# Kernel optimization log

Measured on AMD Instinct MI355X. Metric: run time of the kernel, lower is better.

Reference implementation:

```python
import jax, jax.numpy as jnp
import numpy as np

N = 100000       # nodes
E = 3200000      # edges (avg degree 32)
IN_F = 256
OUT_F = 128
LRELU_ALPHA = 0.2
EPS = 1e-16


def setup_inputs() -> dict:
    key = jax.random.key(0)
    k1, k2, k3, k4 = jax.random.split(key, 4)
    x = jax.random.normal(k1, (N, IN_F), dtype=jnp.float32)
    edge_index = jax.random.randint(k2, (2, E), 0, N, dtype=jnp.int32)
    # xavier_uniform with gain=calculate_gain('relu')=sqrt(2)
    gain = float(np.sqrt(2.0))
    bw = gain * float(np.sqrt(6.0 / (IN_F + OUT_F)))
    weight = jax.random.uniform(k3, (IN_F, OUT_F), dtype=jnp.float32, minval=-bw, maxval=bw)
    ba = gain * float(np.sqrt(6.0 / (1 + 2 * OUT_F)))
    a = jax.random.uniform(k4, (1, 2 * OUT_F), dtype=jnp.float32, minval=-ba, maxval=ba)
    return {"x": x, "edge_index": edge_index, "weight": weight, "a": a}


def reference(x, edge_index, weight, a):
    src = edge_index[0]
    dst = edge_index[1]
    h = x @ weight                                  # [N, OUT_F]
    # e_edge = a @ cat(h[src], h[dst]) == (h @ a_l)[src] + (h @ a_r)[dst]
    a_l = a[0, :OUT_F]
    a_r = a[0, OUT_F:]
    s_l = h @ a_l                                   # [N]
    s_r = h @ a_r                                   # [N]
    e = s_l[src] + s_r[dst]                         # [E]
    e = jnp.where(e >= 0, e, LRELU_ALPHA * e)       # LeakyReLU
    # segment softmax over src groups
    e_max = jax.ops.segment_max(e, src, num_segments=N)   # [N]
    e_exp = jnp.exp(e - e_max[src])                        # [E]
    denom = jax.ops.segment_sum(e_exp, src, num_segments=N)[src] + EPS
    alpha_e = e_exp / denom                                # [E]
    # out[src] += alpha_e * h[dst]  (sparse A_alpha @ h)
    out = jax.ops.segment_sum(alpha_e[:, None] * h[dst], src, num_segments=N)
    return out
```

## Files before the change

kernel.cpp:

```cpp
#include <hip/hip_runtime.h>

#define GN 100000
#define GE 3200000
#define CAP 128
#define NB 391
#define CHUNK 4096
#define BSTRIDE 9216
#define GBLK 782

typedef __attribute__((ext_vector_type(8))) short bf16x8;
typedef __attribute__((ext_vector_type(4))) float f32x4;

__device__ __forceinline__ unsigned short f2bf(float f) {
    unsigned u = __float_as_uint(f);
    u += 0x7fffu + ((u >> 16) & 1u);
    return (unsigned short)(u >> 16);
}
__device__ __forceinline__ unsigned cvtpk(float lo, float hi) {
    unsigned r;
    asm("v_cvt_pk_bf16_f32 %0, %1, %2" : "=v"(r) : "v"(lo), "v"(hi));
    return r;
}

__global__ __launch_bounds__(256) void wprep_kernel(const float* __restrict__ w,
                                                    unsigned short* __restrict__ wT,
                                                    int* __restrict__ bcursor,
                                                    float* __restrict__ s_l) {
    if (blockIdx.x < 32) {
        int flat4 = blockIdx.x * 256 + threadIdx.x;
        int k  = flat4 >> 5;
        int n4 = (flat4 & 31) * 4;
        float4 v = ((const float4*)w)[flat4];
        wT[(size_t)(n4 + 0) * 256 + k] = f2bf(v.x);
        wT[(size_t)(n4 + 1) * 256 + k] = f2bf(v.y);
        wT[(size_t)(n4 + 2) * 256 + k] = f2bf(v.z);
        wT[(size_t)(n4 + 3) * 256 + k] = f2bf(v.w);
    } else if (blockIdx.x < 34) {
        int j = (blockIdx.x - 32) * 256 + threadIdx.x;
        if (j < NB) bcursor[j] = j * BSTRIDE;
    } else {
        int i = (blockIdx.x - 34) * 256 + threadIdx.x;
        if (i < 2 * GN / 4) {
            float4 z = {0.f, 0.f, 0.f, 0.f};
            ((float4*)s_l)[i] = z;
        }
    }
}

__global__ __launch_bounds__(256) void gemmbin_kernel(const float* __restrict__ x,
                                                      const unsigned short* __restrict__ wT,
                                                      const float* __restrict__ a,
                                                      unsigned short* __restrict__ hq,
                                                      float* __restrict__ s_l,
                                                      float* __restrict__ s_r,
                                                      const int* __restrict__ ei,
                                                      int* __restrict__ bcursor,
                                                      unsigned* __restrict__ binned) {
    __shared__ __align__(16) char smem[30848];
    const int half = blockIdx.x >> 1;
    const int tid = threadIdx.x;

    if ((blockIdx.x & 1) == 0) {
        unsigned short (*As)[128][40] = (unsigned short (*)[128][40])smem;
        const int lane = tid & 63, wid = tid >> 6;
        const int l16  = lane & 15, quad = lane >> 4;
        const int wm   = (wid >> 1) * 64, wn = (wid & 1) * 64;
        const int bm   = half * 128;

        f32x4 acc[4][4] = {};

        const int arow = tid >> 1, ahalf = tid & 1;
        int gr = bm + arow; if (gr >= GN) gr = GN - 1;
        const float* xrow = x + (size_t)gr * 256 + ahalf * 16;

        {
            float4 f0 = *(const float4*)(xrow + 0);
            float4 f1 = *(const float4*)(xrow + 4);
            float4 f2 = *(const float4*)(xrow + 8);
            float4 f3 = *(const float4*)(xrow + 12);
            uint4 u0, u1;
            u0.x = cvtpk(f0.x, f0.y); u0.y = cvtpk(f0.z, f0.w);
            u0.z = cvtpk(f1.x, f1.y); u0.w = cvtpk(f1.z, f1.w);
            u1.x = cvtpk(f2.x, f2.y); u1.y = cvtpk(f2.z, f2.w);
            u1.z = cvtpk(f3.x, f3.y); u1.w = cvtpk(f3.z, f3.w);
            *(uint4*)&As[0][arow][ahalf * 16]     = u0;
            *(uint4*)&As[0][arow][ahalf * 16 + 8] = u1;
        }
        bf16x8 bcur[4];
#pragma unroll
        for (int t = 0; t < 4; ++t)
            bcur[t] = *(const bf16x8*)(wT + (size_t)(wn + t * 16 + l16) * 256 + quad * 8);
        __syncthreads();

#pragma unroll
        for (int ks = 0; ks < 8; ++ks) {
            const int cb = ks & 1;
            bf16x8 bnxt[4];
            uint4 u0, u1;
            if (ks < 7) {
                const int k1 = (ks + 1) * 32;
#pragma unroll
                for (int t = 0; t < 4; ++t)
                    bnxt[t] = *(const bf16x8*)(wT + (size_t)(wn + t * 16 + l16) * 256 + k1 + quad * 8);
                float4 f0 = *(const float4*)(xrow + k1);
                float4 f1 = *(const float4*)(xrow + k1 + 4);
                float4 f2 = *(const float4*)(xrow + k1 + 8);
                float4 f3 = *(const float4*)(xrow + k1 + 12);
                u0.x = cvtpk(f0.x, f0.y); u0.y = cvtpk(f0.z, f0.w);
                u0.z = cvtpk(f1.x, f1.y); u0.w = cvtpk(f1.z, f1.w);
                u1.x = cvtpk(f2.x, f2.y); u1.y = cvtpk(f2.z, f2.w);
                u1.z = cvtpk(f3.x, f3.y); u1.w = cvtpk(f3.z, f3.w);
            }
            bf16x8 af[4];
#pragma unroll
            for (int t = 0; t < 4; ++t)
                af[t] = *(const bf16x8*)&As[cb][wm + t * 16 + l16][quad * 8];
#pragma unroll
            for (int ti = 0; ti < 4; ++ti)
#pragma unroll
                for (int tj = 0; tj < 4; ++tj)
                    acc[ti][tj] = __builtin_amdgcn_mfma_f32_16x16x32_bf16(af[ti], bcur[tj], acc[ti][tj], 0, 0, 0);
            if (ks < 7) {
                *(uint4*)&As[cb ^ 1][arow][ahalf * 16]     = u0;
                *(uint4*)&As[cb ^ 1][arow][ahalf * 16 + 8] = u1;
                __syncthreads();
#pragma unroll
                for (int t = 0; t < 4; ++t) bcur[t] = bnxt[t];
            }
        }

        float alv[4], arv[4];
#pragma unroll
        for (int tj = 0; tj < 4; ++tj) {
            alv[tj] = a[wn + tj * 16 + l16];
            arv[tj] = a[128 + wn + tj * 16 + l16];
        }
#pragma unroll
        for (int ti = 0; ti < 4; ++ti) {
            float slp[4], srp[4];
#pragma unroll
            for (int r = 0; r < 4; ++r) {
                int row = bm + wm + ti * 16 + quad * 4 + r;
                float v0 = acc[ti][0][r], v1 = acc[ti][1][r], v2 = acc[ti][2][r], v3 = acc[ti][3][r];
                if (row < GN) {
                    unsigned short* hp = hq + (size_t)row * 128 + wn + l16;
                    hp[0]  = f2bf(v0);
                    hp[16] = f2bf(v1);
                    hp[32] = f2bf(v2);
                    hp[48] = f2bf(v3);
                }
                slp[r] = v0 * alv[0] + v1 * alv[1] + v2 * alv[2] + v3 * alv[3];
                srp[r] = v0 * arv[0] + v1 * arv[1] + v2 * arv[2] + v3 * arv[3];
            }
#pragma unroll
            for (int off = 1; off < 16; off <<= 1)
#pragma unroll
                for (int r = 0; r < 4; ++r) {
                    slp[r] += __shfl_xor(slp[r], off, 64);
                    srp[r] += __shfl_xor(srp[r], off, 64);
                }
            if (l16 == 0) {
#pragma unroll
                for (int r = 0; r < 4; ++r) {
                    int row = bm + wm + ti * 16 + quad * 4 + r;
                    if (row < GN) {
                        atomicAdd(&s_l[row], slp[r]);
                        atomicAdd(&s_r[row], srp[r]);
                    }
                }
            }
        }
    } else {
        int* h_cnt  = (int*)smem;
        int* h_base = h_cnt + NB;
        int* h_gpos = h_base + NB + 1;
        int* h_cur  = h_gpos + NB;
        unsigned* sbuf = (unsigned*)(h_cur + NB);
        unsigned short* sbkt = (unsigned short*)(sbuf + CHUNK);

        const int base = half * CHUNK;
        const int cnt = min(CHUNK, GE - base);

        int srcv[CHUNK / 256], dstv[CHUNK / 256];
#pragma unroll
        for (int i = 0; i < CHUNK / 256; ++i) {
            int idx = tid + i * 256;
            if (idx < cnt) { srcv[i] = ei[base + idx]; dstv[i] = ei[GE + base + idx]; }
            else srcv[i] = -1;
        }
        for (int j = tid; j < NB; j += 256) h_cnt[j] = 0;
        __syncthreads();
#pragma unroll
        for (int i = 0; i < CHUNK / 256; ++i)
            if (srcv[i] >= 0) atomicAdd(&h_cnt[srcv[i] >> 8], 1);
        __syncthreads();
        if (tid < 64) {
            int carry = 0;
            for (int b0 = 0; b0 < NB; b0 += 64) {
                int idx = b0 + tid;
                int v = (idx < NB) ? h_cnt[idx] : 0;
                int xx = v;
#pragma unroll
                for (int off = 1; off < 64; off <<= 1) {
                    int y = __shfl_up(xx, off, 64);
                    if (tid >= off) xx += y;
                }
                if (idx < NB) h_base[idx] = carry + xx - v;
                carry += __shfl(xx, 63, 64);
            }
            if (tid == 0) h_base[NB] = carry;
        }
        __syncthreads();
        for (int j = tid; j < NB; j += 256) {
            h_cur[j] = h_base[j];
            int c = h_cnt[j];
            if (c) h_gpos[j] = atomicAdd(&bcursor[j], c);
        }
        __syncthreads();
#pragma unroll
        for (int i = 0; i < CHUNK / 256; ++i)
            if (srcv[i] >= 0) {
                int b = srcv[i] >> 8;
                int p = atomicAdd(&h_cur[b], 1);
                sbuf[p] = ((unsigned)(srcv[i] & 255) << 17) | (unsigned)dstv[i];
                sbkt[p] = (unsigned short)b;
            }
        __syncthreads();
        for (int p = tid; p < cnt; p += 256) {
            int b = sbkt[p];
            binned[h_gpos[b] + (p - h_base[b])] = sbuf[p];
        }
    }
}

__global__ __launch_bounds__(1024) void fine_kernel(unsigned* __restrict__ binned,
                                                    const int* __restrict__ bcursor,
                                                    int* __restrict__ rowbeg,
                                                    int* __restrict__ rowend) {
    __shared__ unsigned sedge[BSTRIDE];
    __shared__ int n_cnt[256];
    __shared__ int n_base[256];
    __shared__ int n_cur[256];
    const int b = blockIdx.x;
    const int tid = threadIdx.x;
    const int node0 = b * 256;
    const int nn = min(256, GN - node0);
    const int beg = b * BSTRIDE;
    const int cnt = bcursor[b] - beg;
    if (tid < 256) n_cnt[tid] = 0;
    for (int p = tid; p < cnt; p += 1024) sedge[p] = binned[beg + p];
    __syncthreads();
    for (int p = tid; p < cnt; p += 1024)
        atomicAdd(&n_cnt[sedge[p] >> 17], 1);
    __syncthreads();
    if (tid < 64) {
        int carry = 0;
        for (int b0 = 0; b0 < 256; b0 += 64) {
            int idx = b0 + tid;
            int v = n_cnt[idx];
            int x = v;
#pragma unroll
            for (int off = 1; off < 64; off <<= 1) {
                int y = __shfl_up(x, off, 64);
                if (tid >= off) x += y;
            }
            n_base[idx] = carry + x - v;
            carry += __shfl(x, 63, 64);
        }
    }
    __syncthreads();
    if (tid < nn) {
        rowbeg[node0 + tid] = beg + n_base[tid];
        rowend[node0 + tid] = beg + n_base[tid] + n_cnt[tid];
    }
    if (tid < 256) n_cur[tid] = n_base[tid];
    __syncthreads();
    for (int p = tid; p < cnt; p += 1024) {
        unsigned e = sedge[p];
        int pos = atomicAdd(&n_cur[e >> 17], 1);
        binned[beg + pos] = e & 0x1FFFFu;
    }
}

__global__ __launch_bounds__(256) void aggregate_kernel(const uint4* __restrict__ h4,
                                                        const float* __restrict__ s_l,
                                                        const float* __restrict__ s_r,
                                                        const int* __restrict__ rowbeg,
                                                        const int* __restrict__ rowend,
                                                        const int* __restrict__ adj,
                                                        float* __restrict__ out) {
    __shared__ int   s_dst[4][CAP];
    __shared__ float s_w[4][CAP];
    const int wid = threadIdx.x >> 6, lane = threadIdx.x & 63;
    const int node = blockIdx.x * 4 + wid;
    const int beg = rowbeg[node], end = rowend[node];
    const int deg = end - beg;
    const float sl = s_l[node];

    float m = -1e30f;
    for (int j = lane; j < deg; j += 64) {
        int dst = adj[beg + j];
        float e = sl + s_r[dst];
        e = (e >= 0.f) ? e : 0.2f * e;
        if (j < CAP) { s_dst[wid][j] = dst; s_w[wid][j] = e; }
        m = fmaxf(m, e);
    }
#pragma unroll
    for (int off = 1; off < 64; off <<= 1)
        m = fmaxf(m, __shfl_xor(m, off, 64));
    __syncthreads();

    const int n2 = deg < CAP ? deg : CAP;
    float d = 0.f;
    for (int j = lane; j < n2; j += 64) {
        float w = __expf(s_w[wid][j] - m);
        s_w[wid][j] = w;
        d += w;
    }
    for (int j = CAP + lane; j < deg; j += 64) {
        int dst = adj[beg + j];
        float e = sl + s_r[dst];
        e = (e >= 0.f) ? e : 0.2f * e;
        d += __expf(e - m);
    }
#pragma unroll
    for (int off = 1; off < 64; off <<= 1)
        d += __shfl_xor(d, off, 64);
    const float inv = 1.f / (d + 1e-16f);
    __syncthreads();

    const int fl = lane & 15, grp = lane >> 4;
    f32x4 accA = {0.f, 0.f, 0.f, 0.f}, accB = {0.f, 0.f, 0.f, 0.f};
    int j = 0;
#pragma unroll 2
    for (; j < n2; j += 8) {
        int j0 = j + grp, j1 = j + grp + 4;
        bool a0 = j0 < n2, a1 = j1 < n2;
        int   d0 = s_dst[wid][a0 ? j0 : 0];
        int   d1 = s_dst[wid][a1 ? j1 : 0];
        float w0 = a0 ? s_w[wid][j0] : 0.f;
        float w1 = a1 ? s_w[wid][j1] : 0.f;
        uint4 v0 = h4[(size_t)d0 * 16 + fl];
        uint4 v1 = h4[(size_t)d1 * 16 + fl];
        accA.x += w0 * __uint_as_float(v0.x << 16);
        accA.y += w0 * __uint_as_float(v0.x & 0xffff0000u);
        accA.z += w0 * __uint_as_float(v0.y << 16);
        accA.w += w0 * __uint_as_float(v0.y & 0xffff0000u);
        accB.x += w0 * __uint_as_float(v0.z << 16);
        accB.y += w0 * __uint_as_float(v0.z & 0xffff0000u);
        accB.z += w0 * __uint_as_float(v0.w << 16);
        accB.w += w0 * __uint_as_float(v0.w & 0xffff0000u);
        accA.x += w1 * __uint_as_float(v1.x << 16);
        accA.y += w1 * __uint_as_float(v1.x & 0xffff0000u);
        accA.z += w1 * __uint_as_float(v1.y << 16);
        accA.w += w1 * __uint_as_float(v1.y & 0xffff0000u);
        accB.x += w1 * __uint_as_float(v1.z << 16);
        accB.y += w1 * __uint_as_float(v1.z & 0xffff0000u);
        accB.z += w1 * __uint_as_float(v1.w << 16);
        accB.w += w1 * __uint_as_float(v1.w & 0xffff0000u);
    }
    for (; j < deg; j += 4) {
        int jj = j + grp;
        bool act = jj < deg;
        int dst = act ? adj[beg + jj] : 0;
        float e = sl + s_r[dst];
        e = (e >= 0.f) ? e : 0.2f * e;
        float w = act ? __expf(e - m) : 0.f;
        uint4 v = h4[(size_t)dst * 16 + fl];
        accA.x += w * __uint_as_float(v.x << 16);
        accA.y += w * __uint_as_float(v.x & 0xffff0000u);
        accA.z += w * __uint_as_float(v.y << 16);
        accA.w += w * __uint_as_float(v.y & 0xffff0000u);
        accB.x += w * __uint_as_float(v.z << 16);
        accB.y += w * __uint_as_float(v.z & 0xffff0000u);
        accB.z += w * __uint_as_float(v.w << 16);
        accB.w += w * __uint_as_float(v.w & 0xffff0000u);
    }

#pragma unroll
    for (int off = 16; off < 64; off <<= 1) {
        accA.x += __shfl_xor(accA.x, off, 64);
        accA.y += __shfl_xor(accA.y, off, 64);
        accA.z += __shfl_xor(accA.z, off, 64);
        accA.w += __shfl_xor(accA.w, off, 64);
        accB.x += __shfl_xor(accB.x, off, 64);
        accB.y += __shfl_xor(accB.y, off, 64);
        accB.z += __shfl_xor(accB.z, off, 64);
        accB.w += __shfl_xor(accB.w, off, 64);
    }
    if (lane < 16) {
        float* orow = out + (size_t)node * 128 + fl * 8;
        accA.x *= inv; accA.y *= inv; accA.z *= inv; accA.w *= inv;
        accB.x *= inv; accB.y *= inv; accB.z *= inv; accB.w *= inv;
        *(f32x4*)orow       = accA;
        *(f32x4*)(orow + 4) = accB;
    }
}

extern "C" void kernel_launch(void* const* d_in, const int* in_sizes, int n_in,
                              void* d_out, int out_size, void* d_ws, size_t ws_size,
                              hipStream_t stream) {
    const float* x  = (const float*)d_in[0];
    const int*   ei = (const int*)d_in[1];
    const float* w  = (const float*)d_in[2];
    const float* a  = (const float*)d_in[3];
    float* out = (float*)d_out;

    unsigned short* hq = (unsigned short*)d_ws;
    float* s_l     = (float*)(hq + (size_t)GN * 128);
    float* s_r     = s_l + GN;
    int*   bcursor = (int*)(s_r + GN);
    int*   rowbeg  = bcursor + NB;
    int*   rowend  = rowbeg + GN;
    unsigned* binned = (unsigned*)(rowend + GN);
    unsigned short* wT = (unsigned short*)(binned + (size_t)NB * BSTRIDE);

    wprep_kernel<<<34 + (2 * GN / 4 + 255) / 256, 256, 0, stream>>>(w, wT, bcursor, s_l);
    gemmbin_kernel<<<2 * GBLK, 256, 0, stream>>>(x, wT, a, hq, s_l, s_r, ei, bcursor, binned);
    fine_kernel<<<NB, 1024, 0, stream>>>(binned, bcursor, rowbeg, rowend);
    aggregate_kernel<<<GN / 4, 256, 0, stream>>>((const uint4*)hq, s_l, s_r, rowbeg, rowend,
                                                 (const int*)binned, out);
}
```

Before: 366.5 us.

## Fuse fine-grained CSR sort into aggregation kernel using shared-memory edge lists

```diff
diff --git a/kernel.cpp b/kernel.cpp
--- a/kernel.cpp
+++ b/kernel.cpp
@@ -7,6 +7,7 @@
 #define CHUNK 4096
 #define BSTRIDE 9216
 #define GBLK 782
+#define EPT 18
 
 typedef __attribute__((ext_vector_type(8))) short bf16x8;
 typedef __attribute__((ext_vector_type(4))) float f32x4;
@@ -233,25 +234,35 @@
     }
 }
 
-__global__ __launch_bounds__(1024) void fine_kernel(unsigned* __restrict__ binned,
-                                                    const int* __restrict__ bcursor,
-                                                    int* __restrict__ rowbeg,
-                                                    int* __restrict__ rowend) {
+__global__ __launch_bounds__(512) void aggfine_kernel(const uint4* __restrict__ h4,
+                                                      const float* __restrict__ s_l,
+                                                      const float* __restrict__ s_r,
+                                                      const unsigned* __restrict__ binned,
+                                                      const int* __restrict__ bcursor,
+                                                      float* __restrict__ out) {
     __shared__ unsigned sedge[BSTRIDE];
     __shared__ int n_cnt[256];
     __shared__ int n_base[256];
     __shared__ int n_cur[256];
-    const int b = blockIdx.x;
-    const int tid = threadIdx.x;
+    __shared__ float s_w[8][CAP];
+    const int b    = blockIdx.x;
+    const int tid  = threadIdx.x;
+    const int wid  = tid >> 6, lane = tid & 63;
     const int node0 = b * 256;
-    const int nn = min(256, GN - node0);
-    const int beg = b * BSTRIDE;
-    const int cnt = bcursor[b] - beg;
+    const int beg  = b * BSTRIDE;
+    const int cnt  = min(bcursor[b] - beg, BSTRIDE);
+
+    unsigned ev[EPT];
     if (tid < 256) n_cnt[tid] = 0;
-    for (int p = tid; p < cnt; p += 1024) sedge[p] = binned[beg + p];
     __syncthreads();
-    for (int p = tid; p < cnt; p += 1024)
-        atomicAdd(&n_cnt[sedge[p] >> 17], 1);
+#pragma unroll
+    for (int i = 0; i < EPT; ++i) {
+        int p = tid + i * 512;
+        if (p < cnt) {
+            ev[i] = binned[beg + p];
+            atomicAdd(&n_cnt[ev[i] >> 17], 1);
+        }
+    }
     __syncthreads();
     if (tid < 64) {
         int carry = 0;
@@ -269,131 +280,123 @@
         }
     }
     __syncthreads();
-    if (tid < nn) {
-        rowbeg[node0 + tid] = beg + n_base[tid];
-        rowend[node0 + tid] = beg + n_base[tid] + n_cnt[tid];
-    }
     if (tid < 256) n_cur[tid] = n_base[tid];
     __syncthreads();
-    for (int p = tid; p < cnt; p += 1024) {
-        unsigned e = sedge[p];
-        int pos = atomicAdd(&n_cur[e >> 17], 1);
-        binned[beg + pos] = e & 0x1FFFFu;
-    }
-}
-
-__global__ __launch_bounds__(256) void aggregate_kernel(const uint4* __restrict__ h4,
-                                                        const float* __restrict__ s_l,
-                                                        const float* __restrict__ s_r,
-                                                        const int* __restrict__ rowbeg,
-                                                        const int* __restrict__ rowend,
-                                                        const int* __restrict__ adj,
-                                                        float* __restrict__ out) {
-    __shared__ int   s_dst[4][CAP];
-    __shared__ float s_w[4][CAP];
-    const int wid = threadIdx.x >> 6, lane = threadIdx.x & 63;
-    const int node = blockIdx.x * 4 + wid;
-    const int beg = rowbeg[node], end = rowend[node];
-    const int deg = end - beg;
-    const float sl = s_l[node];
-
-    float m = -1e30f;
-    for (int j = lane; j < deg; j += 64) {
-        int dst = adj[beg + j];
-        float e = sl + s_r[dst];
-        e = (e >= 0.f) ? e : 0.2f * e;
-        if (j < CAP) { s_dst[wid][j] = dst; s_w[wid][j] = e; }
-        m = fmaxf(m, e);
-    }
-#pragma unroll
-    for (int off = 1; off < 64; off <<= 1)
-        m = fmaxf(m, __shfl_xor(m, off, 64));
+#pragma unroll
+    for (int i = 0; i < EPT; ++i) {
+        int p = tid + i * 512;
+        if (p < cnt) {
+            unsigned e = ev[i];
+            int pos = atomicAdd(&n_cur[e >> 17], 1);
+            sedge[pos] = e & 0x1FFFFu;
+        }
+    }
     __syncthreads();
 
-    const int n2 = deg < CAP ? deg : CAP;
-    float d = 0.f;
-    for (int j = lane; j < n2; j += 64) {
-        float w = __expf(s_w[wid][j] - m);
-        s_w[wid][j] = w;
-        d += w;
-    }
-    for (int j = CAP + lane; j < deg; j += 64) {
-        int dst = adj[beg + j];
-        float e = sl + s_r[dst];
-        e = (e >= 0.f) ? e : 0.2f * e;
-        d += __expf(e - m);
-    }
-#pragma unroll
-    for (int off = 1; off < 64; off <<= 1)
-        d += __shfl_xor(d, off, 64);
-    const float inv = 1.f / (d + 1e-16f);
-    __syncthreads();
-
     const int fl = lane & 15, grp = lane >> 4;
-    f32x4 accA = {0.f, 0.f, 0.f, 0.f}, accB = {0.f, 0.f, 0.f, 0.f};
-    int j = 0;
+    for (int k = 0; k < 32; ++k) {
+        const int n = wid * 32 + k;
+        const int node = node0 + n;
+        if (node >= GN) break;
+        const int nb  = n_base[n];
+        const int deg = n_cnt[n];
+        const float sl = s_l[node];
+
+        float m = -1e30f;
+        for (int j = lane; j < deg; j += 64) {
+            int dst = (int)sedge[nb + j];
+            float e = sl + s_r[dst];
+            e = (e >= 0.f) ? e : 0.2f * e;
+            if (j < CAP) s_w[wid][j] = e;
+            m = fmaxf(m, e);
+        }
+#pragma unroll
+        for (int off = 1; off < 64; off <<= 1)
+            m = fmaxf(m, __shfl_xor(m, off, 64));
+
+        const int n2 = deg < CAP ? deg : CAP;
+        float d = 0.f;
+        for (int j = lane; j < n2; j += 64) {
+            float w = __expf(s_w[wid][j] - m);
+            s_w[wid][j] = w;
+            d += w;
+        }
+        for (int j = CAP + lane; j < deg; j += 64) {
+            int dst = (int)sedge[nb + j];
+            float e = sl + s_r[dst];
+            e = (e >= 0.f) ? e : 0.2f * e;
+            d += __expf(e - m);
+        }
+#pragma unroll
+        for (int off = 1; off < 64; off <<= 1)
+            d += __shfl_xor(d, off, 64);
+        const float inv = 1.f / (d + 1e-16f);
+
+        f32x4 accA = {0.f, 0.f, 0.f, 0.f}, accB = {0.f, 0.f, 0.f, 0.f};
+        int j = 0;
 #pragma unroll 2
-    for (; j < n2; j += 8) {
-        int j0 = j + grp, j1 = j + grp + 4;
-        bool a0 = j0 < n2, a1 = j1 < n2;
-        int   d0 = s_dst[wid][a0 ? j0 : 0];
-        int   d1 = s_dst[wid][a1 ? j1 : 0];
-        float w0 = a0 ? s_w[wid][j0] : 0.f;
-        float w1 = a1 ? s_w[wid][j1] : 0.f;
-        uint4 v0 = h4[(size_t)d0 * 16 + fl];
-        uint4 v1 = h4[(size_t)d1 * 16 + fl];
-        accA.x += w0 * __uint_as_float(v0.x << 16);
-        accA.y += w0 * __uint_as_float(v0.x & 0xffff0000u);
-        accA.z += w0 * __uint_as_float(v0.y << 16);
-        accA.w += w0 * __uint_as_float(v0.y & 0xffff0000u);
-        accB.x += w0 * __uint_as_float(v0.z << 16);
-        accB.y += w0 * __uint_as_float(v0.z & 0xffff0000u);
-        accB.z += w0 * __uint_as_float(v0.w << 16);
-        accB.w += w0 * __uint_as_float(v0.w & 0xffff0000u);
-        accA.x += w1 * __uint_as_float(v1.x << 16);
-        accA.y += w1 * __uint_as_float(v1.x & 0xffff0000u);
-        accA.z += w1 * __uint_as_float(v1.y << 16);
-        accA.w += w1 * __uint_as_float(v1.y & 0xffff0000u);
-        accB.x += w1 * __uint_as_float(v1.z << 16);
-        accB.y += w1 * __uint_as_float(v1.z & 0xffff0000u);
-        accB.z += w1 * __uint_as_float(v1.w << 16);
-        accB.w += w1 * __uint_as_float(v1.w & 0xffff0000u);
-    }
-    for (; j < deg; j += 4) {
-        int jj = j + grp;
-        bool act = jj < deg;
-        int dst = act ? adj[beg + jj] : 0;
-        float e = sl + s_r[dst];
-        e = (e >= 0.f) ? e : 0.2f * e;
-        float w = act ? __expf(e - m) : 0.f;
-        uint4 v = h4[(size_t)dst * 16 + fl];
-        accA.x += w * __uint_as_float(v.x << 16);
-        accA.y += w * __uint_as_float(v.x & 0xffff0000u);
-        accA.z += w * __uint_as_float(v.y << 16);
-        accA.w += w * __uint_as_float(v.y & 0xffff0000u);
-        accB.x += w * __uint_as_float(v.z << 16);
-        accB.y += w * __uint_as_float(v.z & 0xffff0000u);
-        accB.z += w * __uint_as_float(v.w << 16);
-        accB.w += w * __uint_as_float(v.w & 0xffff0000u);
-    }
-
-#pragma unroll
-    for (int off = 16; off < 64; off <<= 1) {
-        accA.x += __shfl_xor(accA.x, off, 64);
-        accA.y += __shfl_xor(accA.y, off, 64);
-        accA.z += __shfl_xor(accA.z, off, 64);
-        accA.w += __shfl_xor(accA.w, off, 64);
-        accB.x += __shfl_xor(accB.x, off, 64);
-        accB.y += __shfl_xor(accB.y, off, 64);
-        accB.z += __shfl_xor(accB.z, off, 64);
-        accB.w += __shfl_xor(accB.w, off, 64);
-    }
-    if (lane < 16) {
-        float* orow = out + (size_t)node * 128 + fl * 8;
-        accA.x *= inv; accA.y *= inv; accA.z *= inv; accA.w *= inv;
-        accB.x *= inv; accB.y *= inv; accB.z *= inv; accB.w *= inv;
-        *(f32x4*)orow       = accA;
-        *(f32x4*)(orow + 4) = accB;
+        for (; j < n2; j += 8) {
+            int j0 = j + grp, j1 = j + grp + 4;
+            bool a0 = j0 < n2, a1 = j1 < n2;
+            int   d0 = (int)sedge[nb + (a0 ? j0 : 0)];
+            int   d1 = (int)sedge[nb + (a1 ? j1 : 0)];
+            float w0 = a0 ? s_w[wid][j0] : 0.f;
+            float w1 = a1 ? s_w[wid][j1] : 0.f;
+            uint4 v0 = h4[(size_t)d0 * 16 + fl];
+            uint4 v1 = h4[(size_t)d1 * 16 + fl];
+            accA.x += w0 * __uint_as_float(v0.x << 16);
+            accA.y += w0 * __uint_as_float(v0.x & 0xffff0000u);
+            accA.z += w0 * __uint_as_float(v0.y << 16);
+            accA.w += w0 * __uint_as_float(v0.y & 0xffff0000u);
+            accB.x += w0 * __uint_as_float(v0.z << 16);
+            accB.y += w0 * __uint_as_float(v0.z & 0xffff0000u);
+            accB.z += w0 * __uint_as_float(v0.w << 16);
+            accB.w += w0 * __uint_as_float(v0.w & 0xffff0000u);
+            accA.x += w1 * __uint_as_float(v1.x << 16);
+            accA.y += w1 * __uint_as_float(v1.x & 0xffff0000u);
+            accA.z += w1 * __uint_as_float(v1.y << 16);
+            accA.w += w1 * __uint_as_float(v1.y & 0xffff0000u);
+            accB.x += w1 * __uint_as_float(v1.z << 16);
+            accB.y += w1 * __uint_as_float(v1.z & 0xffff0000u);
+            accB.z += w1 * __uint_as_float(v1.w << 16);
+            accB.w += w1 * __uint_as_float(v1.w & 0xffff0000u);
+        }
+        for (; j < deg; j += 4) {
+            int jj = j + grp;
+            bool act = jj < deg;
+            int dst = (int)sedge[nb + (act ? jj : 0)];
+            float e = sl + s_r[dst];
+            e = (e >= 0.f) ? e : 0.2f * e;
+            float w = act ? __expf(e - m) : 0.f;
+            uint4 v = h4[(size_t)dst * 16 + fl];
+            accA.x += w * __uint_as_float(v.x << 16);
+            accA.y += w * __uint_as_float(v.x & 0xffff0000u);
+            accA.z += w * __uint_as_float(v.y << 16);
+            accA.w += w * __uint_as_float(v.y & 0xffff0000u);
+            accB.x += w * __uint_as_float(v.z << 16);
+            accB.y += w * __uint_as_float(v.z & 0xffff0000u);
+            accB.z += w * __uint_as_float(v.w << 16);
+            accB.w += w * __uint_as_float(v.w & 0xffff0000u);
+        }
+
+#pragma unroll
+        for (int off = 16; off < 64; off <<= 1) {
+            accA.x += __shfl_xor(accA.x, off, 64);
+            accA.y += __shfl_xor(accA.y, off, 64);
+            accA.z += __shfl_xor(accA.z, off, 64);
+            accA.w += __shfl_xor(accA.w, off, 64);
+            accB.x += __shfl_xor(accB.x, off, 64);
+            accB.y += __shfl_xor(accB.y, off, 64);
+            accB.z += __shfl_xor(accB.z, off, 64);
+            accB.w += __shfl_xor(accB.w, off, 64);
+        }
+        if (lane < 16) {
+            float* orow = out + (size_t)node * 128 + fl * 8;
+            accA.x *= inv; accA.y *= inv; accA.z *= inv; accA.w *= inv;
+            accB.x *= inv; accB.y *= inv; accB.z *= inv; accB.w *= inv;
+            *(f32x4*)orow       = accA;
+            *(f32x4*)(orow + 4) = accB;
+        }
     }
 }
 
@@ -410,14 +413,10 @@
     float* s_l     = (float*)(hq + (size_t)GN * 128);
     float* s_r     = s_l + GN;
     int*   bcursor = (int*)(s_r + GN);
-    int*   rowbeg  = bcursor + NB;
-    int*   rowend  = rowbeg + GN;
-    unsigned* binned = (unsigned*)(rowend + GN);
+    unsigned* binned = (unsigned*)(bcursor + NB);
     unsigned short* wT = (unsigned short*)(binned + (size_t)NB * BSTRIDE);
 
     wprep_kernel<<<34 + (2 * GN / 4 + 255) / 256, 256, 0, stream>>>(w, wT, bcursor, s_l);
     gemmbin_kernel<<<2 * GBLK, 256, 0, stream>>>(x, wT, a, hq, s_l, s_r, ei, bcursor, binned);
-    fine_kernel<<<NB, 1024, 0, stream>>>(binned, bcursor, rowbeg, rowend);
-    aggregate_kernel<<<GN / 4, 256, 0, stream>>>((const uint4*)hq, s_l, s_r, rowbeg, rowend,
-                                                 (const int*)binned, out);
-}
+    aggfine_kernel<<<NB, 512, 0, stream>>>((const uint4*)hq, s_l, s_r, binned, bcursor, out);
+}
```

New measurement: 364.2 us. No clear change (-0.6%).
